# Optimization experiments

Hardware: AMD Instinct MI355X
Metric: run time of the kernel (lower is better)

The kernel has to match this reference:

```python
import jax, jax.numpy as jnp
import numpy as np

D = 256        # in_dim == out_dim for both node types
NH = 8         # n_heads
DH = D // NH   # d_over_h = 32
NA = 50000     # nodes of type 'a'
NB = 20000     # nodes of type 'b'
E = 100000     # edges per edge type
MAX_LEN = 27759
LN_EPS = 1e-5


def _rte_table():
    # Fixed (non-trainable) sinusoidal table from RelativeTemporalEncoding
    pos = np.arange(MAX_LEN, dtype=np.float32)[:, None]
    div = np.exp(np.arange(0, D, 2, dtype=np.float32) * (-np.log(10000.0) / D))
    tab = np.zeros((MAX_LEN, D), dtype=np.float32)
    tab[:, 0::2] = np.sin(pos * div) / np.sqrt(D)
    tab[:, 1::2] = np.cos(pos * div) / np.sqrt(D)
    return jnp.asarray(tab)


def setup_inputs() -> dict:
    key = jax.random.key(0)
    ks = jax.random.split(key, 24)
    s = 1.0 / np.sqrt(D)
    sh = 1.0 / np.sqrt(DH)
    inp = {
        "Ha": jax.random.normal(ks[0], (NA, D), jnp.float32),
        "Hb": jax.random.normal(ks[1], (NB, D), jnp.float32),
        "rte_emb": _rte_table(),
        # stacked per-node-type weights, index 0 -> 'a', 1 -> 'b'; torch Linear layout [out, in]
        "Wq": jax.random.normal(ks[2], (2, D, D), jnp.float32) * s,
        "Wk": jax.random.normal(ks[3], (2, D, D), jnp.float32) * s,
        "Wm": jax.random.normal(ks[4], (2, D, D), jnp.float32) * s,
        "Wa": jax.random.normal(ks[5], (2, D, D), jnp.float32) * s,
        "rteW": jax.random.normal(ks[6], (2, D, D), jnp.float32) * s,
        "rteb": jnp.zeros((2, D), jnp.float32),
        "ln_g": jnp.ones((2, D), jnp.float32),
        "ln_b": jnp.zeros((2, D), jnp.float32),
        "res_alpha": jnp.ones((2,), jnp.float32),
        # stacked per-edge-type params, index 0 -> e1 (a->a), 1 -> e2 (b->a), 2 -> e3 (a->b)
        "Watt": jax.random.normal(ks[7], (3, DH, DH), jnp.float32) * sh,
        "Wmsg": jax.random.normal(ks[8], (3, DH, DH), jnp.float32) * sh,
        "prior": jnp.ones((3,), jnp.float32),
        "src1": jax.random.randint(ks[9], (E,), 0, NA, jnp.int32),
        "dst1": jax.random.randint(ks[10], (E,), 0, NA, jnp.int32),
        "t1": jax.random.randint(ks[11], (E,), 1, MAX_LEN, jnp.int32),
        "src2": jax.random.randint(ks[12], (E,), 0, NB, jnp.int32),
        "dst2": jax.random.randint(ks[13], (E,), 0, NA, jnp.int32),
        "t2": jax.random.randint(ks[14], (E,), 1, MAX_LEN, jnp.int32),
        "src3": jax.random.randint(ks[15], (E,), 0, NA, jnp.int32),
        "dst3": jax.random.randint(ks[16], (E,), 0, NB, jnp.int32),
        "t3": jax.random.randint(ks[17], (E,), 1, MAX_LEN, jnp.int32),
    }
    return inp


def _edge_agg(Hs, Hd, src, dst, t, Wk_s, Wm_s, Wq_t, rW, rb, Wa_e, Wm_e, pr, rte_emb, n_dst):
    """Per-edge-type attention + segment softmax + weighted scatter-sum."""
    ne = src.shape[0]
    # RTE on gathered source features: h_src + Linear(emb[27759 - time])
    hs = Hs[src] + rte_emb[MAX_LEN - t] @ rW.T + rb            # [E, D]
    K = (hs @ Wk_s.T).reshape(ne, NH, DH)                       # [E, H, DH]
    Q = (Hd[dst] @ Wq_t.T).reshape(ne, NH, DH)                  # [E, H, DH]
    att = jnp.einsum('ehd,df,ehf->eh', K, Wa_e, Q) * pr / np.sqrt(DH).astype(np.float32)
    msg = jnp.einsum('ehd,df->ehf', (hs @ Wm_s.T).reshape(ne, NH, DH), Wm_e)
    # segment softmax over destination nodes (DGL mailbox softmax)
    amax = jax.lax.stop_gradient(jax.ops.segment_max(att, dst, num_segments=n_dst))
    ex = jnp.exp(att - amax[dst])
    den = jax.ops.segment_sum(ex, dst, num_segments=n_dst)
    w = ex / den[dst]                                           # [E, H]
    agg = jax.ops.segment_sum(w[..., None] * msg, dst, num_segments=n_dst)  # [N, H, DH]
    cnt = jax.ops.segment_sum(jnp.ones((ne,), jnp.float32), dst, num_segments=n_dst)
    return agg, (cnt > 0).astype(jnp.float32)


def _update(agg, Hx, Wa_n, g, b, ra):
    x = jax.nn.elu(agg.reshape(agg.shape[0], -1)) @ Wa_n.T
    alpha = jax.nn.sigmoid(ra)
    u = alpha * x + (1.0 - alpha) * Hx
    mu = jnp.mean(u, axis=-1, keepdims=True)
    var = jnp.var(u, axis=-1, keepdims=True)
    return (u - mu) / jnp.sqrt(var + LN_EPS) * g + b


def reference(Ha, Hb, rte_emb, Wq, Wk, Wm, Wa, rteW, rteb, ln_g, ln_b, res_alpha,
              Watt, Wmsg, prior, src1, dst1, t1, src2, dst2, t2, src3, dst3, t3):
    # e1: a -> a ; e2: b -> a ; e3: a -> b
    agg1, h1 = _edge_agg(Ha, Ha, src1, dst1, t1, Wk[0], Wm[0], Wq[0], rteW[0], rteb[0], Watt[0], Wmsg[0], prior[0], rte_emb, NA)
    agg2, h2 = _edge_agg(Hb, Ha, src2, dst2, t2, Wk[1], Wm[1], Wq[0], rteW[1], rteb[1], Watt[1], Wmsg[1], prior[1], rte_emb, NA)
    agg3, h3 = _edge_agg(Ha, Hb, src3, dst3, t3, Wk[0], Wm[0], Wq[1], rteW[0], rteb[0], Watt[2], Wmsg[2], prior[2], rte_emb, NB)
    # cross_reducer='mean': average over edge types that delivered messages
    agg_a = (agg1 + agg2) / jnp.maximum(h1 + h2, 1.0)[:, None, None]
    agg_b = agg3 / jnp.maximum(h3, 1.0)[:, None, None]
    out_a = _update(agg_a, Ha, Wa[0], ln_g[0], ln_b[0], res_alpha[0])
    out_b = _update(agg_b, Hb, Wa[1], ln_g[1], ln_b[1], res_alpha[1])
    return (out_a, out_b)
```

## Files before the change

### kernel.cpp

```cpp
#include <hip/hip_runtime.h>
#include <hip/hip_bf16.h>
#include <math.h>

typedef __hip_bfloat16 bf16;
typedef __attribute__((ext_vector_type(8))) short bf16x8v;
typedef __attribute__((ext_vector_type(4))) float f32x4;


__device__ __forceinline__ float eluf(float x) { return x > 0.f ? x : (__expf(x) - 1.f); }
__device__ __forceinline__ float b2f(unsigned short u) { return __uint_as_float((unsigned)u << 16); }
__device__ __forceinline__ unsigned short f2b(float f) {
    unsigned u = __float_as_uint(f);
    return (unsigned short)((u + 0x7fffu + ((u >> 16) & 1u)) >> 16);
}
__device__ __forceinline__ void unpack8(uint4 u, float* o) {
    o[0] = __uint_as_float(u.x << 16); o[1] = __uint_as_float(u.x & 0xffff0000u);
    o[2] = __uint_as_float(u.y << 16); o[3] = __uint_as_float(u.y & 0xffff0000u);
    o[4] = __uint_as_float(u.z << 16); o[5] = __uint_as_float(u.z & 0xffff0000u);
    o[6] = __uint_as_float(u.w << 16); o[7] = __uint_as_float(u.w & 0xffff0000u);
}
__device__ __forceinline__ void unpack4(ushort4 u, float* o) {
    o[0] = b2f(u.x); o[1] = b2f(u.y); o[2] = b2f(u.z); o[3] = b2f(u.w);
}

#define ASYNC_LDS16(g, l) \
    __builtin_amdgcn_global_load_lds((const __attribute__((address_space(1))) void*)(g), \
                                     (__attribute__((address_space(3))) void*)(l), 16, 0, 0)

__global__ void conv_multi_kernel(
    const float* s0, bf16* o0, int n0, const float* s1, bf16* o1, int n1,
    const float* s2, bf16* o2, int n2, const float* s3, bf16* o3, int n3,
    const float* s4, bf16* o4, int n4, const float* s5, bf16* o5, int n5,
    int* z0, int nz0, int* z1, int nz1)
{
    if (blockIdx.y == 6) {
        for (int i = blockIdx.x * 256 + threadIdx.x; i < nz0; i += gridDim.x * 256) z0[i] = 0;
        if (blockIdx.x == 0 && threadIdx.x < (unsigned)nz1) z1[threadIdx.x] = 0;
        return;
    }
    const float* sp; bf16* op; int n8;
    switch (blockIdx.y) {
        case 0: sp = s0; op = o0; n8 = n0; break;
        case 1: sp = s1; op = o1; n8 = n1; break;
        case 2: sp = s2; op = o2; n8 = n2; break;
        case 3: sp = s3; op = o3; n8 = n3; break;
        case 4: sp = s4; op = o4; n8 = n4; break;
        default: sp = s5; op = o5; n8 = n5; break;
    }
    for (int i = blockIdx.x * 256 + threadIdx.x; i < n8; i += gridDim.x * 256) {
        const float4* p = (const float4*)(sp + (size_t)i * 8);
        float4 a = p[0], b = p[1];
        uint4 u;
        u.x = (unsigned)f2b(a.x) | ((unsigned)f2b(a.y) << 16);
        u.y = (unsigned)f2b(a.z) | ((unsigned)f2b(a.w) << 16);
        u.z = (unsigned)f2b(b.x) | ((unsigned)f2b(b.y) << 16);
        u.w = (unsigned)f2b(b.z) | ((unsigned)f2b(b.w) << 16);
        *(uint4*)(op + (size_t)i * 8) = u;
    }
}

__global__ void fold6_kernel(const float* __restrict__ Watt, const float* __restrict__ Wmsg,
                             const float* __restrict__ prior,
                             const float* __restrict__ Wq, const float* __restrict__ Wm,
                             bf16* __restrict__ WcatA, bf16* __restrict__ WcatB,
                             float* __restrict__ Wmx1f, float* __restrict__ Wmx2f,
                             float* __restrict__ Wmx3f)
{
    const int g = blockIdx.x >> 8;
    const int i = blockIdx.x & 255;
    const int j = threadIdx.x;
    const int h = i >> 5, r = i & 31;
    const float* A; const float* W; float sc = 1.f; int tr = 0;
    bf16* ob; float* of = nullptr;
    const float isq = 0.17677669529663687f;
    switch (g) {
        case 0: A = Watt;        sc = prior[0] * isq; W = Wq;         ob = WcatA;                       break;
        case 1: A = Watt + 1024; sc = prior[1] * isq; W = Wq;         ob = WcatA + (size_t)256 * 256;   break;
        case 2: A = Watt + 2048; sc = prior[2] * isq; W = Wq + 65536; ob = WcatB;                       break;
        case 3: A = Wmsg;        tr = 1; W = Wm;         ob = WcatA + (size_t)768 * 256;  of = Wmx1f;   break;
        case 4: A = Wmsg + 1024; tr = 1; W = Wm + 65536; ob = WcatB + (size_t)512 * 256;  of = Wmx2f;   break;
        default:A = Wmsg + 2048; tr = 1; W = Wm;         ob = WcatA + (size_t)1024 * 256; of = Wmx3f;   break;
    }
    __shared__ float arow[32];
    if (j < 32) arow[j] = (tr ? A[j * 32 + r] : A[r * 32 + j]) * sc;
    __syncthreads();
    float acc = 0.f;
    for (int k = 0; k < 32; ++k) acc += arow[k] * W[(size_t)(h * 32 + k) * 256 + j];
    ((unsigned short*)ob)[(size_t)i * 256 + j] = f2b(acc);
    if (of) of[(size_t)i * 256 + j] = acc;
}

__global__ void combine5_kernel(const float* __restrict__ Wk,
                                const float* __restrict__ Wmx1f, const float* __restrict__ Wmx2f,
                                const float* __restrict__ Wmx3f,
                                const float* __restrict__ rteW, const float* __restrict__ rteb,
                                bf16* __restrict__ WcatR, float* __restrict__ bcatR)
{
    const int g = blockIdx.x >> 8;
    const int i = blockIdx.x & 255;
    const int j = threadIdx.x;
    const float* Wp; const float* rW; const float* rb; int op;
    switch (g) {
        case 0: Wp = Wk;         rW = rteW;         rb = rteb;       op = 0; break;
        case 1: Wp = Wk + 65536; rW = rteW + 65536; rb = rteb + 256; op = 2; break;
        case 2: Wp = Wmx1f;      rW = rteW;         rb = rteb;       op = 1; break;
        case 3: Wp = Wmx2f;      rW = rteW + 65536; rb = rteb + 256; op = 3; break;
        default:Wp = Wmx3f;      rW = rteW;         rb = rteb;       op = 4; break;
    }
    __shared__ float wrow[256];
    wrow[j] = Wp[i * 256 + j];
    __syncthreads();
    float acc = 0.f;
    for (int k = 0; k < 256; ++k) acc += wrow[k] * rW[k * 256 + j];
    ((unsigned short*)WcatR)[(size_t)(op * 256 + i) * 256 + j] = f2b(acc);
    if (j == 0) {
        float b = 0.f;
        for (int k = 0; k < 256; ++k) b += wrow[k] * rb[k];
        bcatR[op * 256 + i] = b;
    }
}

__device__ __forceinline__ void gemm_body(
    const bf16* __restrict__ A, const bf16* __restrict__ Wcat,
    const float* __restrict__ bcat,
    bf16* C0, bf16* C1, bf16* C2, bf16* C3, bf16* C4,
    int wideMask, int M, int bx, int by, char* As, char* Bs)
{
    const int tid = threadIdx.x;
    const int wid = tid >> 6, lane = tid & 63;
    const size_t row0 = (size_t)bx * 128;
    const int gcol0 = by * 128;
    const int cb = by >> 1;
    const int lcol0 = (by & 1) * 128;
    bf16* Csel = (cb == 0) ? C0 : (cb == 1) ? C1 : (cb == 2) ? C2 : (cb == 3) ? C3 : C4;
    const size_t cstride = ((wideMask >> cb) & 1) ? 512 : 256;
    const int wr = wid >> 1, wc = wid & 1;

    f32x4 zero = {0.f, 0.f, 0.f, 0.f};
    f32x4 acc[4][4];
#pragma unroll
    for (int m = 0; m < 4; ++m)
#pragma unroll
        for (int n = 0; n < 4; ++n) acc[m][n] = zero;

    const int sr = wid * 32 + (lane >> 3);
    const int scc = (lane & 7) << 4;
    const char* Ab = (const char*)A;
    const char* Wb = (const char*)Wcat;

    for (int k0 = 0; k0 < 512; k0 += 128) {
#pragma unroll
        for (int i = 0; i < 4; ++i) {
            const int r = sr + i * 8;
            const int csw = scc ^ ((r & 7) << 4);
            const int ldso = wid * 4096 + i * 1024;
            ASYNC_LDS16(Ab + (row0 + r) * 512 + k0 + csw, As + ldso);
            ASYNC_LDS16(Wb + (size_t)(gcol0 + r) * 512 + k0 + csw, Bs + ldso);
        }
        __syncthreads();
#pragma unroll
        for (int kk = 0; kk < 2; ++kk) {
            bf16x8v a[4], b[4];
            const int cbase = kk * 64 + ((lane >> 4) << 4);
#pragma unroll
            for (int m = 0; m < 4; ++m) {
                const int r = wr * 64 + m * 16 + (lane & 15);
                a[m] = *(const bf16x8v*)(As + r * 128 + (cbase ^ ((r & 7) << 4)));
            }
#pragma unroll
            for (int n = 0; n < 4; ++n) {
                const int r = wc * 64 + n * 16 + (lane & 15);
                b[n] = *(const bf16x8v*)(Bs + r * 128 + (cbase ^ ((r & 7) << 4)));
            }
#pragma unroll
            for (int m = 0; m < 4; ++m)
#pragma unroll
                for (int n = 0; n < 4; ++n)
                    acc[m][n] = __builtin_amdgcn_mfma_f32_16x16x32_bf16(a[m], b[n], acc[m][n], 0, 0, 0);
        }
        __syncthreads();
    }
    const int orow = (lane >> 4) << 2;
    const int ocol = lane & 15;
    float bv[4];
#pragma unroll
    for (int n = 0; n < 4; ++n)
        bv[n] = bcat ? bcat[gcol0 + wc * 64 + n * 16 + ocol] : 0.f;
    unsigned short* Cp = (unsigned short*)Csel;
#pragma unroll
    for (int m = 0; m < 4; ++m) {
#pragma unroll
        for (int j = 0; j < 4; ++j) {
            const size_t row = row0 + wr * 64 + m * 16 + orow + j;
            if ((int)row >= M) continue;
#pragma unroll
            for (int n = 0; n < 4; ++n) {
                const int col = lcol0 + wc * 64 + n * 16 + ocol;
                Cp[row * cstride + col] = f2b(acc[m][n][j] + bv[n]);
            }
        }
    }
}

__global__ __launch_bounds__(256) void gemm3_kernel(
    const bf16* A0, const bf16* W0, const float* bc0,
    bf16* o00, bf16* o01, bf16* o02, bf16* o03, bf16* o04, int mask0, int M0,
    const bf16* A1, const bf16* W1,
    bf16* o10, bf16* o11, bf16* o12, bf16* o13, bf16* o14, int mask1, int M1,
    const bf16* A2, const bf16* W2,
    bf16* o20, bf16* o21, bf16* o22, int mask2, int M2,
    int b0, int b1)
{
    __shared__ __align__(16) char As[16384];
    __shared__ __align__(16) char Bs[16384];
    const int bid = blockIdx.x;
    if (bid < b0) {
        gemm_body(A0, W0, bc0, o00, o01, o02, o03, o04, mask0, M0,
                  bid / 10, bid % 10, As, Bs);
    } else if (bid < b1) {
        const int lid = bid - b0;
        gemm_body(A1, W1, nullptr, o10, o11, o12, o13, o14, mask1, M1,
                  lid / 10, lid % 10, As, Bs);
    } else {
        const int lid = bid - b1;
        gemm_body(A2, W2, nullptr, o20, o21, o22, o22, o22, mask2, M2,
                  lid / 6, lid % 6, As, Bs);
    }
}

__global__ __launch_bounds__(512) void ugemm_ln_kernel(
    const bf16* __restrict__ AG, const bf16* __restrict__ Wp,
    const bf16* __restrict__ Hbf, const float* __restrict__ g,
    const float* __restrict__ b, const float* __restrict__ ra,
    float* __restrict__ out, int M)
{
    __shared__ __align__(16) char As[16384];
    __shared__ __align__(16) char Bs[32768];
    __shared__ float red[128][8];
    const int tid = threadIdx.x;
    const int wid = tid >> 6, lane = tid & 63;
    const int wr = wid >> 2, wc = wid & 3;
    const size_t row0 = (size_t)blockIdx.x * 128;

    f32x4 zero = {0.f, 0.f, 0.f, 0.f};
    f32x4 acc[4][4];
#pragma unroll
    for (int m = 0; m < 4; ++m)
#pragma unroll
        for (int n = 0; n < 4; ++n) acc[m][n] = zero;

    const char* Ab = (const char*)AG;
    const char* Wb = (const char*)Wp;
    for (int k0 = 0; k0 < 512; k0 += 128) {
#pragma unroll
        for (int i = 0; i < 2; ++i) {
            const int r = wid * 16 + i * 8 + (lane >> 3);
            const int csw = ((lane & 7) << 4) ^ ((r & 7) << 4);
            ASYNC_LDS16(Ab + (row0 + r) * 512 + k0 + csw, As + (wid * 16 + i * 8) * 128);
        }
#pragma unroll
        for (int i = 0; i < 4; ++i) {
            const int r = wid * 32 + i * 8 + (lane >> 3);
            const int csw = ((lane & 7) << 4) ^ ((r & 7) << 4);
            ASYNC_LDS16(Wb + (size_t)r * 512 + k0 + csw, Bs + (wid * 32 + i * 8) * 128);
        }
        __syncthreads();
#pragma unroll
        for (int kk = 0; kk < 2; ++kk) {
            bf16x8v a[4], bv[4];
            const int cbase = kk * 64 + ((lane >> 4) << 4);
#pragma unroll
            for (int m = 0; m < 4; ++m) {
                const int r = wr * 64 + m * 16 + (lane & 15);
                a[m] = *(const bf16x8v*)(As + r * 128 + (cbase ^ ((r & 7) << 4)));
            }
#pragma unroll
            for (int n = 0; n < 4; ++n) {
                const int r = wc * 64 + n * 16 + (lane & 15);
                bv[n] = *(const bf16x8v*)(Bs + r * 128 + (cbase ^ ((r & 7) << 4)));
            }
#pragma unroll
            for (int m = 0; m < 4; ++m)
#pragma unroll
                for (int n = 0; n < 4; ++n)
                    acc[m][n] = __builtin_amdgcn_mfma_f32_16x16x32_bf16(a[m], bv[n], acc[m][n], 0, 0, 0);
        }
        __syncthreads();
    }
    const float alpha = 1.f / (1.f + __expf(-ra[0]));
    const float beta = 1.f - alpha;
    const int orow = (lane >> 4) << 2;
    const int ocol = lane & 15;
    float gv[4], bb[4];
#pragma unroll
    for (int n = 0; n < 4; ++n) {
        gv[n] = g[wc * 64 + n * 16 + ocol];
        bb[n] = b[wc * 64 + n * 16 + ocol];
    }
    const unsigned short* Hp = (const unsigned short*)Hbf;
#pragma unroll
    for (int m = 0; m < 4; ++m) {
#pragma unroll
        for (int j = 0; j < 4; ++j) {
            const int rl = wr * 64 + m * 16 + orow + j;
            const size_t grow = row0 + rl;
            float s = 0.f, s2 = 0.f;
#pragma unroll
            for (int n = 0; n < 4; ++n) {
                const int col = wc * 64 + n * 16 + ocol;
                float hv = ((int)grow < M) ? b2f(Hp[grow * 256 + col]) : 0.f;
                float u = alpha * acc[m][n][j] + beta * hv;
                acc[m][n][j] = u;
                s += u; s2 += u * u;
            }
            s += __shfl_xor(s, 1); s2 += __shfl_xor(s2, 1);
            s += __shfl_xor(s, 2); s2 += __shfl_xor(s2, 2);
            s += __shfl_xor(s, 4); s2 += __shfl_xor(s2, 4);
            s += __shfl_xor(s, 8); s2 += __shfl_xor(s2, 8);
            if (ocol == 0) { red[rl][wc] = s; red[rl][4 + wc] = s2; }
        }
    }
    __syncthreads();
#pragma unroll
    for (int m = 0; m < 4; ++m) {
#pragma unroll
        for (int j = 0; j < 4; ++j) {
            const int rl = wr * 64 + m * 16 + orow + j;
            const size_t grow = row0 + rl;
            if ((int)grow >= M) continue;
            float S = red[rl][0] + red[rl][1] + red[rl][2] + red[rl][3];
            float S2 = red[rl][4] + red[rl][5] + red[rl][6] + red[rl][7];
            const float mu = S * 0.00390625f;
            const float var = S2 * 0.00390625f - mu * mu;
            const float inv = rsqrtf(var + 1e-5f);
#pragma unroll
            for (int n = 0; n < 4; ++n) {
                const int col = wc * 64 + n * 16 + ocol;
                out[grow * 256 + col] = (acc[m][n][j] - mu) * inv * gv[n] + bb[n];
            }
        }
    }
}

__global__ void hist3_kernel(const int* __restrict__ d1, const int* __restrict__ d2,
                             const int* __restrict__ d3, int2* __restrict__ m1,
                             int2* __restrict__ m2, int2* __restrict__ m3,
                             int E1, int E2, int E3)
{
    int i = blockIdx.x * 256 + threadIdx.x;
    if (i < E1) atomicAdd(&m1[d1[i]].y, 1);
    else if (i < E1 + E2) atomicAdd(&m2[d2[i - E1]].y, 1);
    else if (i < E1 + E2 + E3) atomicAdd(&m3[d3[i - E1 - E2]].y, 1);
}
__global__ void alloc3b_kernel(int2* __restrict__ meta, int* __restrict__ cursor,
                               int* __restrict__ gtot, int NA, int NB)
{
    const int slot = blockIdx.y;
    const int base = (slot == 0) ? 0 : (slot == 1) ? NA : 2 * NA;
    const int len = (slot == 2) ? NB : NA;
    int i = blockIdx.x * 256 + threadIdx.x;
    if (i >= len) return;
    int* gp = gtot + slot;
    int idx = base + i;
    int s = atomicAdd(gp, meta[idx].y);
    meta[idx].x = s; cursor[idx] = s;
}
__global__ void scatter3_kernel(const int* __restrict__ d1, const int* __restrict__ d2,
                                const int* __restrict__ d3,
                                const int* __restrict__ s1, const int* __restrict__ s2,
                                const int* __restrict__ s3,
                                const int* __restrict__ tv1, const int* __restrict__ tv2,
                                const int* __restrict__ tv3,
                                int* __restrict__ cur1, int* __restrict__ cur2,
                                int* __restrict__ cur3,
                                int2* __restrict__ el1, int2* __restrict__ el2,
                                int2* __restrict__ el3, int E1, int E2, int E3, int ml)
{
    int i = blockIdx.x * 256 + threadIdx.x;
    if (i < E1) {
        int p = atomicAdd(&cur1[d1[i]], 1);
        el1[p] = make_int2(s1[i], ml - tv1[i]);
    } else if (i < E1 + E2) {
        int e = i - E1; int p = atomicAdd(&cur2[d2[e]], 1);
        el2[p] = make_int2(s2[e], ml - tv2[e]);
    } else if (i < E1 + E2 + E3) {
        int e = i - E1 - E2; int p = atomicAdd(&cur3[d3[e]], 1);
        el3[p] = make_int2(s3[e], ml - tv3[e]);
    }
}

__device__ __forceinline__ void epass16(
    const bf16* __restrict__ KM, const bf16* __restrict__ RKM,
    const int2* __restrict__ el, int beg, int num,
    int sx_l, int tt_l,
    const float q[8], int lane,
    float s[8], float& denOut)
{
    float den = 0.f;
    const char* KMb = (const char*)KM + lane * 16;
    const char* RMb = (const char*)RKM + lane * 16;
    auto edge = [&](uint4 km, uint4 rm) {
        float a[8], b[8];
        unpack8(km, a); unpack8(rm, b);
#pragma unroll
        for (int x = 0; x < 8; ++x) a[x] += b[x];
        float p = a[0] * q[0] + a[1] * q[1] + a[2] * q[2] + a[3] * q[3]
                + a[4] * q[4] + a[5] * q[5] + a[6] * q[6] + a[7] * q[7];
        p += __shfl_xor(p, 1); p += __shfl_xor(p, 2);
        float ex = __expf(p);
        float exb = __shfl_xor(ex, 32);
        den += exb;
#pragma unroll
        for (int x = 0; x < 8; ++x) s[x] += exb * a[x];
    };
    for (int c0 = 0; c0 < num; c0 += 64) {
        int nc = num - c0; if (nc > 64) nc = 64;
        if (c0 > 0) {
            sx_l = 0; tt_l = 0;
            if (lane < nc) { int2 e = el[beg + c0 + lane]; sx_l = e.x; tt_l = e.y; }
        }
        for (int i0 = 0; i0 < nc; i0 += 4) {
            const int rem = nc - i0;
            const int a0 = __shfl(sx_l, i0),     b0 = __shfl(tt_l, i0);
            const int a1 = __shfl(sx_l, i0 | 1), b1 = __shfl(tt_l, i0 | 1);
            const int a2 = __shfl(sx_l, i0 | 2), b2 = __shfl(tt_l, i0 | 2);
            const int a3 = __shfl(sx_l, i0 | 3), b3 = __shfl(tt_l, i0 | 3);
            uint4 km0, rm0, km1, rm1, km2, rm2, km3, rm3;
            km0 = *(const uint4*)(KMb + (size_t)a0 * 1024);
            rm0 = *(const uint4*)(RMb + (size_t)b0 * 1024);
            if (rem > 1) {
                km1 = *(const uint4*)(KMb + (size_t)a1 * 1024);
                rm1 = *(const uint4*)(RMb + (size_t)b1 * 1024);
            }
            if (rem > 2) {
                km2 = *(const uint4*)(KMb + (size_t)a2 * 1024);
                rm2 = *(const uint4*)(RMb + (size_t)b2 * 1024);
            }
            if (rem > 3) {
                km3 = *(const uint4*)(KMb + (size_t)a3 * 1024);
                rm3 = *(const uint4*)(RMb + (size_t)b3 * 1024);
            }
            edge(km0, rm0);
            if (rem > 1) edge(km1, rm1);
            if (rem > 2) edge(km2, rm2);
            if (rem > 3) edge(km3, rm3);
        }
    }
    denOut = den;
}

__device__ __forceinline__ void epass8(
    const bf16* __restrict__ Kh, const bf16* __restrict__ RKh,
    const bf16* __restrict__ Mt, const bf16* __restrict__ RMt,
    const int2* __restrict__ el, int beg, int num,
    int sx_l, int tt_l,
    const float q[4], int lane,
    float s[4], float& denOut)
{
    float den = 0.f;
    const char* Kb = (const char*)Kh + lane * 8;
    const char* Rb = (const char*)RKh + lane * 8;
    const char* Mb = (const char*)Mt + lane * 8;
    const char* Ub = (const char*)RMt + lane * 8;
    auto edge = [&](ushort4 kv, ushort4 rv, ushort4 mv, ushort4 uv) {
        float a[4], b[4], m[4], r[4];
        unpack4(kv, a); unpack4(rv, b); unpack4(mv, m); unpack4(uv, r);
        float p = (a[0] + b[0]) * q[0] + (a[1] + b[1]) * q[1]
                + (a[2] + b[2]) * q[2] + (a[3] + b[3]) * q[3];
        p += __shfl_xor(p, 1); p += __shfl_xor(p, 2); p += __shfl_xor(p, 4);
        float ex = __expf(p);
        den += ex;
#pragma unroll
        for (int x = 0; x < 4; ++x) s[x] += ex * (m[x] + r[x]);
    };
    for (int c0 = 0; c0 < num; c0 += 64) {
        int nc = num - c0; if (nc > 64) nc = 64;
        if (c0 > 0) {
            sx_l = 0; tt_l = 0;
            if (lane < nc) { int2 e = el[beg + c0 + lane]; sx_l = e.x; tt_l = e.y; }
        }
        for (int i0 = 0; i0 < nc; i0 += 4) {
            const int rem = nc - i0;
            const int a0 = __shfl(sx_l, i0),     b0 = __shfl(tt_l, i0);
            const int a1 = __shfl(sx_l, i0 | 1), b1 = __shfl(tt_l, i0 | 1);
            const int a2 = __shfl(sx_l, i0 | 2), b2 = __shfl(tt_l, i0 | 2);
            const int a3 = __shfl(sx_l, i0 | 3), b3 = __shfl(tt_l, i0 | 3);
            ushort4 k0, r0, m0, u0, k1, r1, m1, u1, k2, r2, m2, u2, k3, r3, m3, u3;
            k0 = *(const ushort4*)(Kb + (size_t)a0 * 1024);
            r0 = *(const ushort4*)(Rb + (size_t)b0 * 1024);
            m0 = *(const ushort4*)(Mb + (size_t)a0 * 512);
            u0 = *(const ushort4*)(Ub + (size_t)b0 * 512);
            if (rem > 1) {
                k1 = *(const ushort4*)(Kb + (size_t)a1 * 1024);
                r1 = *(const ushort4*)(Rb + (size_t)b1 * 1024);
                m1 = *(const ushort4*)(Mb + (size_t)a1 * 512);
                u1 = *(const ushort4*)(Ub + (size_t)b1 * 512);
            }
            if (rem > 2) {
                k2 = *(const ushort4*)(Kb + (size_t)a2 * 1024);
                r2 = *(const ushort4*)(Rb + (size_t)b2 * 1024);
                m2 = *(const ushort4*)(Mb + (size_t)a2 * 512);
                u2 = *(const ushort4*)(Ub + (size_t)b2 * 512);
            }
            if (rem > 3) {
                k3 = *(const ushort4*)(Kb + (size_t)a3 * 1024);
                r3 = *(const ushort4*)(Rb + (size_t)b3 * 1024);
                m3 = *(const ushort4*)(Mb + (size_t)a3 * 512);
                u3 = *(const ushort4*)(Ub + (size_t)b3 * 512);
            }
            edge(k0, r0, m0, u0);
            if (rem > 1) edge(k1, r1, m1, u1);
            if (rem > 2) edge(k2, r2, m2, u2);
            if (rem > 3) edge(k3, r3, m3, u3);
        }
    }
    denOut = den;
}

__global__ __launch_bounds__(256) void edge_fused_kernel(
    const bf16* __restrict__ Qa1, const bf16* __restrict__ Qa2,
    const bf16* __restrict__ KMa1, const bf16* __restrict__ RKM1,
    const int2* __restrict__ meta1, const int2* __restrict__ el1,
    const bf16* __restrict__ KMb, const bf16* __restrict__ RKM2,
    const int2* __restrict__ meta2, const int2* __restrict__ el2,
    bf16* __restrict__ AGa, int NA,
    const bf16* __restrict__ Qb3, const bf16* __restrict__ Ma3, const bf16* __restrict__ RM3p,
    const int2* __restrict__ meta3, const int2* __restrict__ el3,
    bf16* __restrict__ AGb, int NB, int nbblk)
{
    const int wid = threadIdx.x >> 6, lane = threadIdx.x & 63;
    if ((int)blockIdx.x >= nbblk) {
        const int n = ((int)blockIdx.x - nbblk) * 4 + wid;
        if (n >= NA) return;
        const int2 m1 = meta1[n], m2 = meta2[n];
        const int beg1 = m1.x, num1 = m1.y, beg2 = m2.x, num2 = m2.y;
        int sx1 = 0, tt1 = 0, sx2 = 0, tt2 = 0;
        if (lane < (num1 < 64 ? num1 : 64)) { int2 e = el1[beg1 + lane]; sx1 = e.x; tt1 = e.y; }
        if (lane < (num2 < 64 ? num2 : 64)) { int2 e = el2[beg2 + lane]; sx2 = e.x; tt2 = e.y; }
        float q1[8];
        unpack8(*(const uint4*)(Qa1 + (size_t)n * 256 + (lane & 31) * 8), q1);
        const uint4 qv2 = *(const uint4*)(Qa2 + (size_t)n * 256 + (lane & 31) * 8);
        float sf[8] = {0.f, 0.f, 0.f, 0.f, 0.f, 0.f, 0.f, 0.f};
        float s[8], den;
        if (num1 > 0) {
#pragma unroll
            for (int x = 0; x < 8; ++x) s[x] = 0.f;
            epass16(KMa1, RKM1, el1, beg1, num1, sx1, tt1, q1, lane, s, den);
            float invd = 1.f / den;
#pragma unroll
            for (int x = 0; x < 8; ++x) sf[x] += s[x] * invd;
        }
        if (num2 > 0) {
            float q2[8];
            unpack8(qv2, q2);
#pragma unroll
            for (int x = 0; x < 8; ++x) s[x] = 0.f;
            epass16(KMb, RKM2, el2, beg2, num2, sx2, tt2, q2, lane, s, den);
            float invd = 1.f / den;
#pragma unroll
            for (int x = 0; x < 8; ++x) sf[x] += s[x] * invd;
        }
        float dv = 1.f / fmaxf((float)((num1 > 0) + (num2 > 0)), 1.f);
        if (lane >= 32) {
            uint4 o;
            o.x = (unsigned)f2b(eluf(sf[0] * dv)) | ((unsigned)f2b(eluf(sf[1] * dv)) << 16);
            o.y = (unsigned)f2b(eluf(sf[2] * dv)) | ((unsigned)f2b(eluf(sf[3] * dv)) << 16);
            o.z = (unsigned)f2b(eluf(sf[4] * dv)) | ((unsigned)f2b(eluf(sf[5] * dv)) << 16);
            o.w = (unsigned)f2b(eluf(sf[6] * dv)) | ((unsigned)f2b(eluf(sf[7] * dv)) << 16);
            *(uint4*)((unsigned short*)AGa + (size_t)n * 256 + (lane - 32) * 8) = o;
        }
    } else {
        const int n = (int)blockIdx.x * 4 + wid;
        if (n >= NB) return;
        const int2 m3 = meta3[n];
        const int beg3 = m3.x, num3 = m3.y;
        int sx3 = 0, tt3 = 0;
        if (lane < (num3 < 64 ? num3 : 64)) { int2 e = el3[beg3 + lane]; sx3 = e.x; tt3 = e.y; }
        float q3[4];
        unpack4(*(const ushort4*)(Qb3 + (size_t)n * 256 + lane * 4), q3);
        float s[4] = {0.f, 0.f, 0.f, 0.f};
        float den = 1.f;
        if (num3 > 0) {
            epass8(KMa1, RKM1, Ma3, RM3p, el3, beg3, num3, sx3, tt3, q3, lane, s, den);
            float invd = 1.f / den;
#pragma unroll
            for (int x = 0; x < 4; ++x) s[x] *= invd;
        }
        ushort4 o;
        o.x = f2b(eluf(s[0])); o.y = f2b(eluf(s[1]));
        o.z = f2b(eluf(s[2])); o.w = f2b(eluf(s[3]));
        *(ushort4*)((unsigned short*)AGb + (size_t)n * 256 + lane * 4) = o;
    }
}

extern "C" void kernel_launch(void* const* d_in, const int* in_sizes, int n_in,
                              void* d_out, int out_size, void* d_ws, size_t ws_size,
                              hipStream_t stream)
{
    const float* Ha   = (const float*)d_in[0];
    const float* Hb   = (const float*)d_in[1];
    const float* rte  = (const float*)d_in[2];
    const float* Wq   = (const float*)d_in[3];
    const float* Wk   = (const float*)d_in[4];
    const float* Wm   = (const float*)d_in[5];
    const float* Wa   = (const float*)d_in[6];
    const float* rteW = (const float*)d_in[7];
    const float* rteb = (const float*)d_in[8];
    const float* ln_g = (const float*)d_in[9];
    const float* ln_b = (const float*)d_in[10];
    const float* ra   = (const float*)d_in[11];
    const float* Watt = (const float*)d_in[12];
    const float* Wmsg = (const float*)d_in[13];
    const float* prior= (const float*)d_in[14];
    const int* src1 = (const int*)d_in[15];
    const int* dst1 = (const int*)d_in[16];
    const int* t1   = (const int*)d_in[17];
    const int* src2 = (const int*)d_in[18];
    const int* dst2 = (const int*)d_in[19];
    const int* t2   = (const int*)d_in[20];
    const int* src3 = (const int*)d_in[21];
    const int* dst3 = (const int*)d_in[22];
    const int* t3   = (const int*)d_in[23];

    const int NA = in_sizes[0] / 256;
    const int NB = in_sizes[1] / 256;
    const int ML = in_sizes[2] / 256;
    const int E1 = in_sizes[15];
    const int E2 = in_sizes[18];
    const int E3 = in_sizes[21];
    const int NAp = (NA + 127) & ~127;
    const int NBp = (NB + 127) & ~127;
    const int MLp = (ML + 127) & ~127;

    char* w = (char*)d_ws;
    size_t off = 0;
    auto alloc = [&](size_t bytes) -> void* {
        void* p = w + off;
        off += (bytes + 511) & ~(size_t)511;
        return p;
    };
    bf16* WcatA = (bf16*)alloc((size_t)1280 * 256 * 2);
    bf16* WcatB = (bf16*)alloc((size_t)768 * 256 * 2);
    bf16* WcatR = (bf16*)alloc((size_t)1280 * 256 * 2);
    float* bcatR = (float*)alloc(1280 * 4);
    bf16* Wa_bf = (bf16*)alloc(131072 * 2);
    float* Wmx1f = (float*)alloc(65536 * 4);
    float* Wmx2f = (float*)alloc(65536 * 4);
    float* Wmx3f = (float*)alloc(65536 * 4);
    bf16* Ha_bf = (bf16*)alloc((size_t)NAp * 512);
    bf16* Hb_bf = (bf16*)alloc((size_t)NBp * 512);
    bf16* rte_bf = (bf16*)alloc((size_t)MLp * 512);
    bf16* Qa1 = (bf16*)alloc((size_t)NAp * 512);
    bf16* Qa2 = (bf16*)alloc((size_t)NAp * 512);
    bf16* KMa1 = (bf16*)alloc((size_t)NAp * 1024);
    bf16* RKM1 = (bf16*)alloc((size_t)MLp * 1024);
    bf16* RKM2 = (bf16*)alloc((size_t)MLp * 1024);
    bf16* RM3p = (bf16*)alloc((size_t)MLp * 512);
    int2* meta = (int2*)alloc((size_t)(NA + NA + NB) * 8);
    int2* meta1 = meta, *meta2 = meta + NA, *meta3 = meta + 2 * NA;
    int* curb = (int*)alloc((size_t)(NA + NA + NB) * 4);
    int* cur1 = curb, *cur2 = curb + NA, *cur3 = curb + 2 * NA;
    int2* elist1 = (int2*)alloc((size_t)E1 * 8);
    int2* elist2 = (int2*)alloc((size_t)E2 * 8);
    int2* elist3 = (int2*)alloc((size_t)E3 * 8);
    int* gtot = (int*)alloc(16);
    bf16* Ma3 = (bf16*)d_out;
    bf16* Qb3 = (bf16*)d_out + (size_t)NAp * 256;
    bf16* KMb = (bf16*)d_out + (size_t)NAp * 256 + (size_t)NBp * 256;
    bf16* AGa = Qa1;
    bf16* AGb = Qb3;

    conv_multi_kernel<<<dim3(512, 7), 256, 0, stream>>>(
        Ha, Ha_bf, NA * 32, Hb, Hb_bf, NB * 32, rte, rte_bf, ML * 32,
        Wa, Wa_bf, 16384,
        Wk, WcatA + (size_t)512 * 256, 8192,
        Wk + 65536, WcatB + (size_t)256 * 256, 8192,
        (int*)meta, 2 * (NA + NA + NB), gtot, 4);
    fold6_kernel<<<1536, 256, 0, stream>>>(Watt, Wmsg, prior, Wq, Wm,
                                           WcatA, WcatB, Wmx1f, Wmx2f, Wmx3f);
    combine5_kernel<<<1280, 256, 0, stream>>>(Wk, Wmx1f, Wmx2f, Wmx3f, rteW, rteb, WcatR, bcatR);

    int Etot = E1 + E2 + E3;
    hist3_kernel<<<dim3((Etot + 255) / 256), 256, 0, stream>>>(dst1, dst2, dst3, meta1, meta2, meta3, E1, E2, E3);
    alloc3b_kernel<<<dim3((NA + 255) / 256, 3), 256, 0, stream>>>(meta, curb, gtot, NA, NB);
    scatter3_kernel<<<dim3((Etot + 255) / 256), 256, 0, stream>>>(
        dst1, dst2, dst3, src1, src2, src3, t1, t2, t3,
        cur1, cur2, cur3, elist1, elist2, elist3, E1, E2, E3, ML);

    const int nx0 = MLp / 128, nx1 = NAp / 128, nx2 = NBp / 128;
    const int b0 = nx0 * 10;
    const int b1 = b0 + nx1 * 10;
    const int btot = b1 + nx2 * 6;
    gemm3_kernel<<<dim3(btot), 256, 0, stream>>>(
        rte_bf, WcatR, bcatR, RKM1, RKM1 + 256, RKM2, RKM2 + 256, RM3p, 0xF, ML,
        Ha_bf, WcatA, Qa1, Qa2, KMa1, KMa1 + 256, Ma3, 0xC, NA,
        Hb_bf, WcatB, Qb3, KMb, KMb + 256, 0x6, NB,
        b0, b1);

    const int nablk = (NA + 3) / 4;
    const int nbblk = (NB + 3) / 4;
    edge_fused_kernel<<<dim3(nablk + nbblk), 256, 0, stream>>>(
        Qa1, Qa2, KMa1, RKM1, meta1, elist1,
        KMb, RKM2, meta2, elist2,
        AGa, NA,
        Qb3, Ma3, RM3p, meta3, elist3,
        AGb, NB, nbblk);

    float* out = (float*)d_out;
    ugemm_ln_kernel<<<dim3(NBp / 128), 512, 0, stream>>>(
        AGb, Wa_bf + 65536, Hb_bf, ln_g + 256, ln_b + 256, ra + 1,
        out + (size_t)NA * 256, NB);
    ugemm_ln_kernel<<<dim3(NAp / 128), 512, 0, stream>>>(
        AGa, Wa_bf, Ha_bf, ln_g, ln_b, ra, out, NA);
}
```

Measured before the change: 378.3 us.

## Merge CSR build kernels into weight-fold and GEMM launches, add XCD-aware block remap

The histogram, offset-allocation and scatter kernels that build per-destination edge lists are folded into the fold6, combine5 and gemm3 launches as extra blocks. Three separate launches disappear and their small, latency-bound work can run alongside the weight-prep and GEMM blocks. The GEMM blocks are also renumbered so that consecutive logical tiles land on the same XCD, which is meant to improve L2 reuse of the shared weight and A tiles. A scatter block may be delayed behind GEMM blocks in the same launch, and the remap formula depends on blocks being dispatched round-robin across 8 XCDs.

```diff
diff --git a/kernel.cpp b/kernel.cpp
--- a/kernel.cpp
+++ b/kernel.cpp
@@ -59,13 +59,24 @@
     }
 }
 
-__global__ void fold6_kernel(const float* __restrict__ Watt, const float* __restrict__ Wmsg,
-                             const float* __restrict__ prior,
-                             const float* __restrict__ Wq, const float* __restrict__ Wm,
-                             bf16* __restrict__ WcatA, bf16* __restrict__ WcatB,
-                             float* __restrict__ Wmx1f, float* __restrict__ Wmx2f,
-                             float* __restrict__ Wmx3f)
-{
+__global__ void fold6hist_kernel(const float* __restrict__ Watt, const float* __restrict__ Wmsg,
+                                 const float* __restrict__ prior,
+                                 const float* __restrict__ Wq, const float* __restrict__ Wm,
+                                 bf16* __restrict__ WcatA, bf16* __restrict__ WcatB,
+                                 float* __restrict__ Wmx1f, float* __restrict__ Wmx2f,
+                                 float* __restrict__ Wmx3f,
+                                 const int* __restrict__ d1, const int* __restrict__ d2,
+                                 const int* __restrict__ d3, int2* __restrict__ m1,
+                                 int2* __restrict__ m2, int2* __restrict__ m3,
+                                 int E1, int E2, int E3)
+{
+    if (blockIdx.x >= 1536) {
+        int i = ((int)blockIdx.x - 1536) * 256 + threadIdx.x;
+        if (i < E1) atomicAdd(&m1[d1[i]].y, 1);
+        else if (i < E1 + E2) atomicAdd(&m2[d2[i - E1]].y, 1);
+        else if (i < E1 + E2 + E3) atomicAdd(&m3[d3[i - E1 - E2]].y, 1);
+        return;
+    }
     const int g = blockIdx.x >> 8;
     const int i = blockIdx.x & 255;
     const int j = threadIdx.x;
@@ -90,12 +101,27 @@
     if (of) of[(size_t)i * 256 + j] = acc;
 }
 
-__global__ void combine5_kernel(const float* __restrict__ Wk,
-                                const float* __restrict__ Wmx1f, const float* __restrict__ Wmx2f,
-                                const float* __restrict__ Wmx3f,
-                                const float* __restrict__ rteW, const float* __restrict__ rteb,
-                                bf16* __restrict__ WcatR, float* __restrict__ bcatR)
-{
+__global__ void comb5alloc_kernel(const float* __restrict__ Wk,
+                                  const float* __restrict__ Wmx1f, const float* __restrict__ Wmx2f,
+                                  const float* __restrict__ Wmx3f,
+                                  const float* __restrict__ rteW, const float* __restrict__ rteb,
+                                  bf16* __restrict__ WcatR, float* __restrict__ bcatR,
+                                  int2* __restrict__ meta, int* __restrict__ cursor,
+                                  int* __restrict__ gtot, int NA, int NB, int bps)
+{
+    if (blockIdx.x >= 1280) {
+        const int lid = (int)blockIdx.x - 1280;
+        const int slot = lid / bps;
+        const int base = (slot == 0) ? 0 : (slot == 1) ? NA : 2 * NA;
+        const int len = (slot == 2) ? NB : NA;
+        int i = (lid % bps) * 256 + threadIdx.x;
+        if (i >= len) return;
+        int* gp = gtot + slot;
+        int idx = base + i;
+        int s = atomicAdd(gp, meta[idx].y);
+        meta[idx].x = s; cursor[idx] = s;
+        return;
+    }
     const int g = blockIdx.x >> 8;
     const int i = blockIdx.x & 255;
     const int j = threadIdx.x;
@@ -202,27 +228,51 @@
     }
 }
 
-__global__ __launch_bounds__(256) void gemm3_kernel(
+__global__ __launch_bounds__(256) void gemm3s_kernel(
     const bf16* A0, const bf16* W0, const float* bc0,
     bf16* o00, bf16* o01, bf16* o02, bf16* o03, bf16* o04, int mask0, int M0,
     const bf16* A1, const bf16* W1,
     bf16* o10, bf16* o11, bf16* o12, bf16* o13, bf16* o14, int mask1, int M1,
     const bf16* A2, const bf16* W2,
     bf16* o20, bf16* o21, bf16* o22, int mask2, int M2,
-    int b0, int b1)
+    int b0, int b1, int btot, int scB,
+    const int* __restrict__ d1, const int* __restrict__ d2, const int* __restrict__ d3,
+    const int* __restrict__ s1, const int* __restrict__ s2, const int* __restrict__ s3,
+    const int* __restrict__ tv1, const int* __restrict__ tv2, const int* __restrict__ tv3,
+    int* __restrict__ cur1, int* __restrict__ cur2, int* __restrict__ cur3,
+    int2* __restrict__ el1, int2* __restrict__ el2, int2* __restrict__ el3,
+    int E1, int E2, int E3, int ml)
 {
     __shared__ __align__(16) char As[16384];
     __shared__ __align__(16) char Bs[16384];
     const int bid = blockIdx.x;
-    if (bid < b0) {
+    if (bid < scB) {
+        int i = bid * 256 + threadIdx.x;
+        if (i < E1) {
+            int p = atomicAdd(&cur1[d1[i]], 1);
+            el1[p] = make_int2(s1[i], ml - tv1[i]);
+        } else if (i < E1 + E2) {
+            int e = i - E1; int p = atomicAdd(&cur2[d2[e]], 1);
+            el2[p] = make_int2(s2[e], ml - tv2[e]);
+        } else if (i < E1 + E2 + E3) {
+            int e = i - E1 - E2; int p = atomicAdd(&cur3[d3[e]], 1);
+            el3[p] = make_int2(s3[e], ml - tv3[e]);
+        }
+        return;
+    }
+    const int g = bid - scB;
+    const int q = btot >> 3, r = btot & 7;
+    const int xcd = g & 7, idx = g >> 3;
+    const int lbid = (xcd < r ? xcd * (q + 1) : r * (q + 1) + (xcd - r) * q) + idx;
+    if (lbid < b0) {
         gemm_body(A0, W0, bc0, o00, o01, o02, o03, o04, mask0, M0,
-                  bid / 10, bid % 10, As, Bs);
-    } else if (bid < b1) {
-        const int lid = bid - b0;
+                  lbid / 10, lbid % 10, As, Bs);
+    } else if (lbid < b1) {
+        const int lid = lbid - b0;
         gemm_body(A1, W1, nullptr, o10, o11, o12, o13, o14, mask1, M1,
                   lid / 10, lid % 10, As, Bs);
     } else {
-        const int lid = bid - b1;
+        const int lid = lbid - b1;
         gemm_body(A2, W2, nullptr, o20, o21, o22, o22, o22, mask2, M2,
                   lid / 6, lid % 6, As, Bs);
     }
@@ -339,53 +389,6 @@
                 out[grow * 256 + col] = (acc[m][n][j] - mu) * inv * gv[n] + bb[n];
             }
         }
-    }
-}
-
-__global__ void hist3_kernel(const int* __restrict__ d1, const int* __restrict__ d2,
-                             const int* __restrict__ d3, int2* __restrict__ m1,
-                             int2* __restrict__ m2, int2* __restrict__ m3,
-                             int E1, int E2, int E3)
-{
-    int i = blockIdx.x * 256 + threadIdx.x;
-    if (i < E1) atomicAdd(&m1[d1[i]].y, 1);
-    else if (i < E1 + E2) atomicAdd(&m2[d2[i - E1]].y, 1);
-    else if (i < E1 + E2 + E3) atomicAdd(&m3[d3[i - E1 - E2]].y, 1);
-}
-__global__ void alloc3b_kernel(int2* __restrict__ meta, int* __restrict__ cursor,
-                               int* __restrict__ gtot, int NA, int NB)
-{
-    const int slot = blockIdx.y;
-    const int base = (slot == 0) ? 0 : (slot == 1) ? NA : 2 * NA;
-    const int len = (slot == 2) ? NB : NA;
-    int i = blockIdx.x * 256 + threadIdx.x;
-    if (i >= len) return;
-    int* gp = gtot + slot;
-    int idx = base + i;
-    int s = atomicAdd(gp, meta[idx].y);
-    meta[idx].x = s; cursor[idx] = s;
-}
-__global__ void scatter3_kernel(const int* __restrict__ d1, const int* __restrict__ d2,
-                                const int* __restrict__ d3,
-                                const int* __restrict__ s1, const int* __restrict__ s2,
-                                const int* __restrict__ s3,
-                                const int* __restrict__ tv1, const int* __restrict__ tv2,
-                                const int* __restrict__ tv3,
-                                int* __restrict__ cur1, int* __restrict__ cur2,
-                                int* __restrict__ cur3,
-                                int2* __restrict__ el1, int2* __restrict__ el2,
-                                int2* __restrict__ el3, int E1, int E2, int E3, int ml)
-{
-    int i = blockIdx.x * 256 + threadIdx.x;
-    if (i < E1) {
-        int p = atomicAdd(&cur1[d1[i]], 1);
-        el1[p] = make_int2(s1[i], ml - tv1[i]);
-    } else if (i < E1 + E2) {
-        int e = i - E1; int p = atomicAdd(&cur2[d2[e]], 1);
-        el2[p] = make_int2(s2[e], ml - tv2[e]);
-    } else if (i < E1 + E2 + E3) {
-        int e = i - E1 - E2; int p = atomicAdd(&cur3[d3[e]], 1);
-        el3[p] = make_int2(s3[e], ml - tv3[e]);
     }
 }
 
@@ -670,32 +673,36 @@
     bf16* AGa = Qa1;
     bf16* AGb = Qb3;
 
+    const int Etot = E1 + E2 + E3;
+    const int histB = (Etot + 255) / 256;
+    const int bps = (((NA > NB ? NA : NB) + 255) / 256);
+
     conv_multi_kernel<<<dim3(512, 7), 256, 0, stream>>>(
         Ha, Ha_bf, NA * 32, Hb, Hb_bf, NB * 32, rte, rte_bf, ML * 32,
         Wa, Wa_bf, 16384,
         Wk, WcatA + (size_t)512 * 256, 8192,
         Wk + 65536, WcatB + (size_t)256 * 256, 8192,
         (int*)meta, 2 * (NA + NA + NB), gtot, 4);
-    fold6_kernel<<<1536, 256, 0, stream>>>(Watt, Wmsg, prior, Wq, Wm,
-                                           WcatA, WcatB, Wmx1f, Wmx2f, Wmx3f);
-    combine5_kernel<<<1280, 256, 0, stream>>>(Wk, Wmx1f, Wmx2f, Wmx3f, rteW, rteb, WcatR, bcatR);
-
-    int Etot = E1 + E2 + E3;
-    hist3_kernel<<<dim3((Etot + 255) / 256), 256, 0, stream>>>(dst1, dst2, dst3, meta1, meta2, meta3, E1, E2, E3);
-    alloc3b_kernel<<<dim3((NA + 255) / 256, 3), 256, 0, stream>>>(meta, curb, gtot, NA, NB);
-    scatter3_kernel<<<dim3((Etot + 255) / 256), 256, 0, stream>>>(
-        dst1, dst2, dst3, src1, src2, src3, t1, t2, t3,
-        cur1, cur2, cur3, elist1, elist2, elist3, E1, E2, E3, ML);
+
+    fold6hist_kernel<<<1536 + histB, 256, 0, stream>>>(
+        Watt, Wmsg, prior, Wq, Wm, WcatA, WcatB, Wmx1f, Wmx2f, Wmx3f,
+        dst1, dst2, dst3, meta1, meta2, meta3, E1, E2, E3);
+
+    comb5alloc_kernel<<<1280 + bps * 3, 256, 0, stream>>>(
+        Wk, Wmx1f, Wmx2f, Wmx3f, rteW, rteb, WcatR, bcatR,
+        meta, curb, gtot, NA, NB, bps);
 
     const int nx0 = MLp / 128, nx1 = NAp / 128, nx2 = NBp / 128;
     const int b0 = nx0 * 10;
     const int b1 = b0 + nx1 * 10;
     const int btot = b1 + nx2 * 6;
-    gemm3_kernel<<<dim3(btot), 256, 0, stream>>>(
+    gemm3s_kernel<<<dim3(histB + btot), 256, 0, stream>>>(
         rte_bf, WcatR, bcatR, RKM1, RKM1 + 256, RKM2, RKM2 + 256, RM3p, 0xF, ML,
         Ha_bf, WcatA, Qa1, Qa2, KMa1, KMa1 + 256, Ma3, 0xC, NA,
         Hb_bf, WcatB, Qb3, KMb, KMb + 256, 0x6, NB,
-        b0, b1);
+        b0, b1, btot, histB,
+        dst1, dst2, dst3, src1, src2, src3, t1, t2, t3,
+        cur1, cur2, cur3, elist1, elist2, elist3, E1, E2, E3, ML);
 
     const int nablk = (NA + 3) / 4;
     const int nbblk = (NB + 3) / 4;
```

Measured after the change: 366.0 us. 1.03x faster.
